# Kernel optimization log

Measured on AMD Instinct MI355X. Metric: run time of the kernel, lower is better.

The kernel has to match this reference:

```python
import jax, jax.numpy as jnp
import numpy as np

B, N, D, K = 16, 65536, 24, 512
ATTRACTION_WEIGHT = 1.0
REPULSION_WEIGHT = 1.5
MARGIN_WEIGHT = 5.0
THRESHOLD = 0.5
MARGIN = 0.2
TAU = 0.7


def setup_inputs() -> dict:
    key = jax.random.key(0)
    k1, k2, k3 = jax.random.split(key, 3)
    beta = jax.random.normal(k1, (B, N, 1), jnp.float32)
    embed = jax.random.normal(k2, (B, N, D), jnp.float32)
    # First K hits of each event are the condensation points (one per instance),
    # remaining hits get a random instance id in [0, K).
    rand_sid = jax.random.randint(k3, (B, N - K), 0, K, jnp.int32)
    cp_sid = jnp.broadcast_to(jnp.arange(K, dtype=jnp.int32), (B, K))
    slice_id = jnp.concatenate([cp_sid, rand_sid], axis=1)
    is_cp = jnp.concatenate(
        [jnp.ones((B, K), jnp.int32), jnp.zeros((B, N - K), jnp.int32)], axis=1)
    return {"beta": beta, "embed": embed, "slice_id": slice_id, "is_cp": is_cp}


def _per_batch(beta_b, emb_b, sid, cp):
    # beta_b: [N], emb_b: [N, D], sid: [N] int, cp: [N] int
    n = beta_b.shape[0]
    f32 = beta_b.dtype
    cp_mask = cp == 1
    pos_count = cp_mask.sum()
    neg_count = n - pos_count

    seg_cnt = jax.ops.segment_sum(jnp.ones((n,), f32), sid, num_segments=K)
    inst_present = seg_cnt > 0
    cp_per_inst = jax.ops.segment_sum(cp_mask.astype(f32), sid, num_segments=K)
    valid_inst = inst_present & (cp_per_inst == 1)  # inst_cp.sum() == 1

    # --- grouped softmax CE over each instance (temperature TAU) ---
    logits = jnp.clip(beta_b, -20.0, 20.0) / TAU
    seg_max = jax.ops.segment_max(logits, sid, num_segments=K)
    safe_max = jnp.where(inst_present, seg_max, 0.0)
    ex = jnp.exp(logits - safe_max[sid])
    denom = jax.ops.segment_sum(ex, sid, num_segments=K)
    cp_logit = jax.ops.segment_sum(jnp.where(cp_mask, logits, 0.0), sid,
                                   num_segments=K)  # exactly one cp when valid
    p_cp = jnp.exp(cp_logit - safe_max) / jnp.maximum(denom, 1e-30)
    loss_inst = -jnp.log(p_cp + 1e-9)
    slice_count = valid_inst.sum()
    beta_slice_ce = jnp.where(valid_inst, loss_inst, 0.0).sum() / jnp.maximum(slice_count, 1)

    # --- margin loss on sigmoid(beta) ---
    beta_prob = jax.nn.sigmoid(jnp.clip(beta_b, -20.0, 20.0))
    pos_m = jnp.where(cp_mask, jax.nn.relu(THRESHOLD + MARGIN - beta_prob), 0.0).sum() \
        / jnp.maximum(pos_count, 1)
    neg_m = jnp.where(cp_mask, 0.0, jax.nn.relu(beta_prob - (THRESHOLD - MARGIN))).sum() \
        / jnp.maximum(neg_count, 1)
    beta_loss = beta_slice_ce + MARGIN_WEIGHT * (pos_m + neg_m)

    # --- attraction: hits pulled to first CP of their instance ---
    idx = jnp.arange(n, dtype=jnp.int32)
    first_cp = jax.ops.segment_min(jnp.where(cp_mask, idx, n), sid, num_segments=K)
    has_cp = (first_cp < n) & inst_present
    cp_emb = emb_b[jnp.minimum(first_cp, n - 1)]  # [K, D]
    d2 = jnp.minimum(((emb_b - cp_emb[sid]) ** 2).sum(-1), 50.0)
    d2_mean = jax.ops.segment_sum(d2, sid, num_segments=K) / jnp.maximum(seg_cnt, 1.0)
    attraction = ATTRACTION_WEIGHT * jnp.where(has_cp, d2_mean, 0.0).sum()

    # --- repulsion: pairwise exp(-d2) between CP embeddings (incl. diagonal) ---
    m = has_cp.astype(f32)
    mcount = m.sum()
    sq = (cp_emb ** 2).sum(-1)
    pd2 = sq[:, None] + sq[None, :] - 2.0 * (cp_emb @ cp_emb.T)
    pd2 = jnp.clip(pd2, 0.0, 50.0)
    rep = (jnp.exp(-pd2) * (m[:, None] * m[None, :])).sum() / jnp.maximum(mcount * mcount, 1.0)
    repulsion = jnp.where(mcount > 1, REPULSION_WEIGHT * rep, 0.0)

    valid = (pos_count >= 1) & (neg_count >= 1) & (slice_count > 0)
    total = beta_loss + attraction + repulsion
    return total, beta_loss, attraction, repulsion, valid


def reference(beta, embed, slice_id, is_cp):
    beta = jnp.nan_to_num(jnp.squeeze(beta, -1), nan=0.0, posinf=0.0, neginf=0.0)
    embed = jnp.nan_to_num(embed, nan=0.0, posinf=0.0, neginf=0.0)
    total, bl, al, rl, valid = jax.vmap(_per_batch)(beta, embed, slice_id, is_cp)
    v = valid.astype(beta.dtype)
    count = v.sum()
    safe = jnp.maximum(count, 1.0)
    ok = count > 0
    final = jnp.where(ok, (total * v).sum() / safe, 0.0)
    beta_log = jnp.where(ok, (bl * v).sum() / safe, 0.0)
    attr_log = jnp.where(ok, (al * v).sum() / safe, 0.0)
    repl_log = jnp.where(ok, (rl * v).sum() / safe, 0.0)
    return final, beta_log, attr_log, repl_log
```

## Files before the change

kernel.cpp:

```cpp
#include <hip/hip_runtime.h>
#include <math.h>

#define BB 16
#define NN 65536
#define DD 24
#define KK 512
#define CH 64
#define HPB (NN / CH)
#define TPB 256
#define RPB 4
#define GB (KK / RPB)

__device__ __forceinline__ float fixnum(float v) {
  return __builtin_isfinite(v) ? v : 0.0f;
}

__device__ __forceinline__ float blockReduceSum(float v, float* sbuf) {
  __syncthreads();
  #pragma unroll
  for (int off = 32; off > 0; off >>= 1) v += __shfl_down(v, off, 64);
  int wid = threadIdx.x >> 6, lane = threadIdx.x & 63;
  if (lane == 0) sbuf[wid] = v;
  __syncthreads();
  return sbuf[0] + sbuf[1] + sbuf[2] + sbuf[3];
}

__global__ __launch_bounds__(TPB) void k1_seg(
    const float* __restrict__ beta, const int* __restrict__ sid,
    const int* __restrict__ iscp,
    float* __restrict__ cnt_part, float* __restrict__ den_part,
    float* __restrict__ cp_cnt, float* __restrict__ cp_logit,
    int* __restrict__ first_cp, float* __restrict__ margin)
{
  __shared__ float s_cnt[KK];
  __shared__ float s_den[KK];
  __shared__ float sred[4];
  int b = blockIdx.x / CH, c = blockIdx.x % CH, t = threadIdx.x;
  for (int k = t; k < KK; k += TPB) { s_cnt[k] = 0.f; s_den[k] = 0.f; }
  __syncthreads();
  float pm = 0.f, nm = 0.f;
  #pragma unroll
  for (int i = 0; i < HPB / TPB; ++i) {
    int h = c * HPB + i * TPB + t;
    size_t g = (size_t)b * NN + h;
    float bv = fixnum(beta[g]);
    float bc = fminf(fmaxf(bv, -20.f), 20.f);
    float logit = bc / 0.7f;
    int s = sid[g];
    atomicAdd(&s_cnt[s], 1.0f);
    atomicAdd(&s_den[s], expf(logit));
    float prob = 1.0f / (1.0f + expf(-bc));
    if (iscp[g] == 1) {
      atomicAdd(&cp_cnt[b * KK + s], 1.0f);
      atomicAdd(&cp_logit[b * KK + s], logit);
      atomicMin(&first_cp[b * KK + s], h);
      pm += fmaxf(0.7f - prob, 0.f);
    } else {
      nm += fmaxf(prob - 0.3f, 0.f);
    }
  }
  float pms = blockReduceSum(pm, sred);
  float nms = blockReduceSum(nm, sred);
  if (t == 0) { atomicAdd(&margin[2 * b], pms); atomicAdd(&margin[2 * b + 1], nms); }
  __syncthreads();
  for (int k = t; k < KK; k += TPB) {
    cnt_part[((size_t)b * CH + c) * KK + k] = s_cnt[k];
    den_part[((size_t)b * CH + c) * KK + k] = s_den[k];
  }
}

__global__ __launch_bounds__(TPB) void k2_fin(
    const float* __restrict__ embed,
    const float* __restrict__ cnt_part, const float* __restrict__ den_part,
    const float* __restrict__ cp_cnt, const float* __restrict__ cp_logit,
    const int* __restrict__ first_cp,
    float* __restrict__ seg_cnt, float* __restrict__ loss_v,
    float* __restrict__ valid_f, float* __restrict__ has_cp_f,
    float* __restrict__ cp_emb)
{
  int idx = blockIdx.x * TPB + threadIdx.x;
  if (idx >= BB * KK) return;
  int b = idx / KK, k = idx - b * KK;
  float cnt = 0.f, den = 0.f;
  for (int c = 0; c < CH; ++c) {
    cnt += cnt_part[((size_t)b * CH + c) * KK + k];
    den += den_part[((size_t)b * CH + c) * KK + k];
  }
  bool present = cnt > 0.f;
  bool vinst = present && (cp_cnt[idx] == 1.0f);
  float p = expf(cp_logit[idx]) / fmaxf(den, 1e-30f);
  float loss = -logf(p + 1e-9f);
  loss_v[idx] = vinst ? loss : 0.f;
  valid_f[idx] = vinst ? 1.f : 0.f;
  int fc = first_cp[idx];
  has_cp_f[idx] = ((fc < NN) && present) ? 1.f : 0.f;
  seg_cnt[idx] = cnt;
  int row = fc < NN ? fc : NN - 1;
  const float4* src = (const float4*)(embed + ((size_t)b * NN + row) * DD);
  float4* dst = (float4*)(cp_emb + (size_t)idx * DD);
  #pragma unroll
  for (int q = 0; q < DD / 4; ++q) {
    float4 v = src[q];
    v.x = fixnum(v.x); v.y = fixnum(v.y); v.z = fixnum(v.z); v.w = fixnum(v.w);
    dst[q] = v;
  }
}

__global__ __launch_bounds__(TPB) void k3_attr(
    const float* __restrict__ embed, const int* __restrict__ sid,
    const float* __restrict__ cp_emb, float* __restrict__ d2_part)
{
  __shared__ float s_ce[KK * DD];
  __shared__ float s_d2[KK];
  int b = blockIdx.x / CH, c = blockIdx.x % CH, t = threadIdx.x;
  const float4* src = (const float4*)(cp_emb + (size_t)b * KK * DD);
  float4* dst = (float4*)s_ce;
  for (int i = t; i < KK * DD / 4; i += TPB) dst[i] = src[i];
  for (int k = t; k < KK; k += TPB) s_d2[k] = 0.f;
  __syncthreads();
  #pragma unroll
  for (int i = 0; i < HPB / TPB; ++i) {
    int h = c * HPB + i * TPB + t;
    size_t g = (size_t)b * NN + h;
    const float4* e = (const float4*)(embed + g * DD);
    int s = sid[g];
    const float4* ce = (const float4*)(s_ce + s * DD);
    float d2 = 0.f;
    #pragma unroll
    for (int q = 0; q < DD / 4; ++q) {
      float4 ev = e[q]; float4 cv = ce[q];
      float x;
      x = fixnum(ev.x) - cv.x; d2 += x * x;
      x = fixnum(ev.y) - cv.y; d2 += x * x;
      x = fixnum(ev.z) - cv.z; d2 += x * x;
      x = fixnum(ev.w) - cv.w; d2 += x * x;
    }
    atomicAdd(&s_d2[s], fminf(d2, 50.f));
  }
  __syncthreads();
  for (int k = t; k < KK; k += TPB)
    d2_part[((size_t)b * CH + c) * KK + k] = s_d2[k];
}

__global__ __launch_bounds__(TPB) void k3b_rep(
    const float* __restrict__ cp_emb, const float* __restrict__ has_cp_f,
    float* __restrict__ rep_sum)
{
  __shared__ float sred[4];
  int b = blockIdx.x / GB;
  int r0 = (blockIdx.x % GB) * RPB;
  int t = threadIdx.x;
  int j0 = t, j1 = t + TPB;
  const float* base = cp_emb + (size_t)b * KK * DD;
  float cj0[DD], cj1[DD];
  #pragma unroll
  for (int d = 0; d < DD; ++d) { cj0[d] = base[j0 * DD + d]; cj1[d] = base[j1 * DD + d]; }
  float m0 = has_cp_f[b * KK + j0], m1 = has_cp_f[b * KK + j1];
  float acc = 0.f;
  for (int ri = 0; ri < RPB; ++ri) {
    int i = r0 + ri;
    float mi = has_cp_f[b * KK + i];
    float d20 = 0.f, d21 = 0.f;
    #pragma unroll
    for (int d = 0; d < DD; ++d) {
      float ci = base[i * DD + d];
      float x0 = ci - cj0[d]; d20 += x0 * x0;
      float x1 = ci - cj1[d]; d21 += x1 * x1;
    }
    acc += mi * (m0 * expf(-fminf(d20, 50.f)) + m1 * expf(-fminf(d21, 50.f)));
  }
  float tot = blockReduceSum(acc, sred);
  if (t == 0) atomicAdd(&rep_sum[b], tot);
}

__global__ __launch_bounds__(TPB) void k4_batch(
    const float* __restrict__ d2_part, const float* __restrict__ seg_cnt,
    const float* __restrict__ loss_v, const float* __restrict__ valid_f,
    const float* __restrict__ cp_cnt, const float* __restrict__ has_cp_f,
    const float* __restrict__ margin, const float* __restrict__ rep_sum,
    float* __restrict__ batch_out)
{
  __shared__ float sred[4];
  int b = blockIdx.x, t = threadIdx.x;
  float attr = 0.f, ce = 0.f, vcnt = 0.f, pcnt = 0.f, mcnt = 0.f;
  for (int k = t; k < KK; k += TPB) {
    float ds = 0.f;
    for (int c = 0; c < CH; ++c) ds += d2_part[((size_t)b * CH + c) * KK + k];
    int idx = b * KK + k;
    float cnt = seg_cnt[idx];
    float hc = has_cp_f[idx];
    attr += hc * (ds / fmaxf(cnt, 1.f));
    ce += loss_v[idx];
    vcnt += valid_f[idx];
    pcnt += cp_cnt[idx];
    mcnt += hc;
  }
  attr = blockReduceSum(attr, sred);
  ce   = blockReduceSum(ce, sred);
  vcnt = blockReduceSum(vcnt, sred);
  pcnt = blockReduceSum(pcnt, sred);
  mcnt = blockReduceSum(mcnt, sred);
  if (t == 0) {
    float pos = pcnt, neg = (float)NN - pos;
    float slice_ce = ce / fmaxf(vcnt, 1.f);
    float pm = margin[2 * b] / fmaxf(pos, 1.f);
    float nm = margin[2 * b + 1] / fmaxf(neg, 1.f);
    float beta_loss = slice_ce + 5.0f * (pm + nm);
    float rep = rep_sum[b] / fmaxf(mcnt * mcnt, 1.f);
    float repulsion = (mcnt > 1.f) ? 1.5f * rep : 0.f;
    float valid = (pos >= 1.f && neg >= 1.f && vcnt > 0.f) ? 1.f : 0.f;
    batch_out[b * 8 + 0] = beta_loss + attr + repulsion;
    batch_out[b * 8 + 1] = beta_loss;
    batch_out[b * 8 + 2] = attr;
    batch_out[b * 8 + 3] = repulsion;
    batch_out[b * 8 + 4] = valid;
  }
}

__global__ void k5_final(const float* __restrict__ batch_out, float* __restrict__ out) {
  if (threadIdx.x == 0 && blockIdx.x == 0) {
    float s0 = 0.f, s1 = 0.f, s2 = 0.f, s3 = 0.f, c = 0.f;
    for (int b = 0; b < BB; ++b) {
      float v = batch_out[b * 8 + 4];
      c  += v;
      s0 += batch_out[b * 8 + 0] * v;
      s1 += batch_out[b * 8 + 1] * v;
      s2 += batch_out[b * 8 + 2] * v;
      s3 += batch_out[b * 8 + 3] * v;
    }
    float safe = fmaxf(c, 1.f);
    bool ok = c > 0.f;
    out[0] = ok ? s0 / safe : 0.f;
    out[1] = ok ? s1 / safe : 0.f;
    out[2] = ok ? s2 / safe : 0.f;
    out[3] = ok ? s3 / safe : 0.f;
  }
}

extern "C" void kernel_launch(void* const* d_in, const int* in_sizes, int n_in,
                              void* d_out, int out_size, void* d_ws, size_t ws_size,
                              hipStream_t stream) {
  (void)in_sizes; (void)n_in; (void)out_size; (void)ws_size;
  const float* beta  = (const float*)d_in[0];
  const float* embed = (const float*)d_in[1];
  const int*   sid   = (const int*)d_in[2];
  const int*   iscp  = (const int*)d_in[3];
  float* out = (float*)d_out;
  char* ws = (char*)d_ws;

  size_t off = 0;
  auto alloc = [&](size_t bytes) {
    size_t o = off; off += (bytes + 255) & ~(size_t)255; return o;
  };
  const size_t BKf = (size_t)BB * KK * 4;
  size_t o_cp_cnt  = alloc(BKf);
  size_t o_cp_lg   = alloc(BKf);
  size_t o_margin  = alloc((size_t)BB * 2 * 4);
  size_t o_rep     = alloc((size_t)BB * 4);
  size_t zero_end  = off;
  size_t o_first   = alloc(BKf);
  size_t o_cnt_p   = alloc((size_t)BB * CH * KK * 4);
  size_t o_den_p   = alloc((size_t)BB * CH * KK * 4);
  size_t o_d2_p    = alloc((size_t)BB * CH * KK * 4);
  size_t o_cpe     = alloc((size_t)BB * KK * DD * 4);
  size_t o_segc    = alloc(BKf);
  size_t o_lossv   = alloc(BKf);
  size_t o_validf  = alloc(BKf);
  size_t o_hascp   = alloc(BKf);
  size_t o_bout    = alloc((size_t)BB * 8 * 4);

  hipMemsetAsync(ws, 0, zero_end, stream);
  hipMemsetAsync(ws + o_first, 0x7f, BKf, stream);

  k1_seg<<<BB * CH, TPB, 0, stream>>>(beta, sid, iscp,
      (float*)(ws + o_cnt_p), (float*)(ws + o_den_p),
      (float*)(ws + o_cp_cnt), (float*)(ws + o_cp_lg),
      (int*)(ws + o_first), (float*)(ws + o_margin));

  k2_fin<<<(BB * KK) / TPB, TPB, 0, stream>>>(embed,
      (const float*)(ws + o_cnt_p), (const float*)(ws + o_den_p),
      (const float*)(ws + o_cp_cnt), (const float*)(ws + o_cp_lg),
      (const int*)(ws + o_first),
      (float*)(ws + o_segc), (float*)(ws + o_lossv), (float*)(ws + o_validf),
      (float*)(ws + o_hascp), (float*)(ws + o_cpe));

  k3_attr<<<BB * CH, TPB, 0, stream>>>(embed, sid,
      (const float*)(ws + o_cpe), (float*)(ws + o_d2_p));

  k3b_rep<<<BB * GB, TPB, 0, stream>>>((const float*)(ws + o_cpe),
      (const float*)(ws + o_hascp), (float*)(ws + o_rep));

  k4_batch<<<BB, TPB, 0, stream>>>((const float*)(ws + o_d2_p),
      (const float*)(ws + o_segc), (const float*)(ws + o_lossv),
      (const float*)(ws + o_validf), (const float*)(ws + o_cp_cnt),
      (const float*)(ws + o_hascp), (const float*)(ws + o_margin),
      (const float*)(ws + o_rep), (float*)(ws + o_bout));

  k5_final<<<1, 64, 0, stream>>>((const float*)(ws + o_bout), out);
}
```

Before: 244.3 us.

## Fuse attraction and repulsion kernels, drop memsets and global atomics

```diff
diff --git a/kernel.cpp b/kernel.cpp
--- a/kernel.cpp
+++ b/kernel.cpp
@@ -8,8 +8,7 @@
 #define CH 64
 #define HPB (NN / CH)
 #define TPB 256
-#define RPB 4
-#define GB (KK / RPB)
+#define RPB 8
 
 __device__ __forceinline__ float fixnum(float v) {
   return __builtin_isfinite(v) ? v : 0.0f;
@@ -28,32 +27,39 @@
 __global__ __launch_bounds__(TPB) void k1_seg(
     const float* __restrict__ beta, const int* __restrict__ sid,
     const int* __restrict__ iscp,
-    float* __restrict__ cnt_part, float* __restrict__ den_part,
-    float* __restrict__ cp_cnt, float* __restrict__ cp_logit,
-    int* __restrict__ first_cp, float* __restrict__ margin)
+    float* __restrict__ cnt_p, float* __restrict__ den_p,
+    float* __restrict__ cpc_p, float* __restrict__ cpl_p,
+    int* __restrict__ first_p, float* __restrict__ marg_p)
 {
-  __shared__ float s_cnt[KK];
-  __shared__ float s_den[KK];
+  __shared__ float s_cnt[KK], s_den[KK], s_cpc[KK], s_cpl[KK];
+  __shared__ int   s_first[KK];
   __shared__ float sred[4];
-  int b = blockIdx.x / CH, c = blockIdx.x % CH, t = threadIdx.x;
-  for (int k = t; k < KK; k += TPB) { s_cnt[k] = 0.f; s_den[k] = 0.f; }
-  __syncthreads();
+  int b = blockIdx.x >> 6, c = blockIdx.x & 63, t = threadIdx.x;
+  for (int k = t; k < KK; k += TPB) {
+    s_cnt[k] = 0.f; s_den[k] = 0.f; s_cpc[k] = 0.f; s_cpl[k] = 0.f; s_first[k] = NN;
+  }
+  __syncthreads();
+  int h0 = c * HPB + t * 4;
+  size_t g0 = (size_t)b * NN + h0;
+  float4 bv = *(const float4*)(beta + g0);
+  int4   sv = *(const int4*)(sid + g0);
+  int4   cv = *(const int4*)(iscp + g0);
   float pm = 0.f, nm = 0.f;
-  #pragma unroll
-  for (int i = 0; i < HPB / TPB; ++i) {
-    int h = c * HPB + i * TPB + t;
-    size_t g = (size_t)b * NN + h;
-    float bv = fixnum(beta[g]);
-    float bc = fminf(fmaxf(bv, -20.f), 20.f);
-    float logit = bc / 0.7f;
-    int s = sid[g];
+  float bs[4] = {bv.x, bv.y, bv.z, bv.w};
+  int   ss[4] = {sv.x, sv.y, sv.z, sv.w};
+  int   cs[4] = {cv.x, cv.y, cv.z, cv.w};
+  #pragma unroll
+  for (int j = 0; j < 4; ++j) {
+    float bc = fminf(fmaxf(fixnum(bs[j]), -20.f), 20.f);
+    float logit = bc * (1.0f / 0.7f);
+    int s = ss[j];
     atomicAdd(&s_cnt[s], 1.0f);
-    atomicAdd(&s_den[s], expf(logit));
-    float prob = 1.0f / (1.0f + expf(-bc));
-    if (iscp[g] == 1) {
-      atomicAdd(&cp_cnt[b * KK + s], 1.0f);
-      atomicAdd(&cp_logit[b * KK + s], logit);
-      atomicMin(&first_cp[b * KK + s], h);
+    atomicAdd(&s_den[s], __expf(logit));
+    float prob = 1.0f / (1.0f + __expf(-bc));
+    if (cs[j] == 1) {
+      atomicAdd(&s_cpc[s], 1.0f);
+      atomicAdd(&s_cpl[s], logit);
+      atomicMin(&s_first[s], h0 + j);
       pm += fmaxf(0.7f - prob, 0.f);
     } else {
       nm += fmaxf(prob - 0.3f, 0.f);
@@ -61,40 +67,47 @@
   }
   float pms = blockReduceSum(pm, sred);
   float nms = blockReduceSum(nm, sred);
-  if (t == 0) { atomicAdd(&margin[2 * b], pms); atomicAdd(&margin[2 * b + 1], nms); }
-  __syncthreads();
+  if (t == 0) { marg_p[2 * blockIdx.x] = pms; marg_p[2 * blockIdx.x + 1] = nms; }
+  __syncthreads();
+  size_t base = ((size_t)b * CH + c) * KK;
   for (int k = t; k < KK; k += TPB) {
-    cnt_part[((size_t)b * CH + c) * KK + k] = s_cnt[k];
-    den_part[((size_t)b * CH + c) * KK + k] = s_den[k];
+    cnt_p[base + k] = s_cnt[k]; den_p[base + k] = s_den[k];
+    cpc_p[base + k] = s_cpc[k]; cpl_p[base + k] = s_cpl[k];
+    first_p[base + k] = s_first[k];
   }
 }
 
 __global__ __launch_bounds__(TPB) void k2_fin(
     const float* __restrict__ embed,
-    const float* __restrict__ cnt_part, const float* __restrict__ den_part,
-    const float* __restrict__ cp_cnt, const float* __restrict__ cp_logit,
-    const int* __restrict__ first_cp,
+    const float* __restrict__ cnt_p, const float* __restrict__ den_p,
+    const float* __restrict__ cpc_p, const float* __restrict__ cpl_p,
+    const int* __restrict__ first_p,
     float* __restrict__ seg_cnt, float* __restrict__ loss_v,
     float* __restrict__ valid_f, float* __restrict__ has_cp_f,
-    float* __restrict__ cp_emb)
+    float* __restrict__ cpc_tot, float* __restrict__ cp_emb,
+    float* __restrict__ d2_acc, float* __restrict__ rep_acc)
 {
   int idx = blockIdx.x * TPB + threadIdx.x;
-  if (idx >= BB * KK) return;
-  int b = idx / KK, k = idx - b * KK;
-  float cnt = 0.f, den = 0.f;
+  int b = idx >> 9, k = idx & (KK - 1);
+  float cnt = 0.f, den = 0.f, cpc = 0.f, cpl = 0.f;
+  int fc = NN;
+  #pragma unroll 8
   for (int c = 0; c < CH; ++c) {
-    cnt += cnt_part[((size_t)b * CH + c) * KK + k];
-    den += den_part[((size_t)b * CH + c) * KK + k];
+    size_t base = ((size_t)b * CH + c) * KK + k;
+    cnt += cnt_p[base]; den += den_p[base];
+    cpc += cpc_p[base]; cpl += cpl_p[base];
+    fc = min(fc, first_p[base]);
   }
   bool present = cnt > 0.f;
-  bool vinst = present && (cp_cnt[idx] == 1.0f);
-  float p = expf(cp_logit[idx]) / fmaxf(den, 1e-30f);
-  float loss = -logf(p + 1e-9f);
-  loss_v[idx] = vinst ? loss : 0.f;
+  bool vinst = present && (cpc == 1.0f);
+  float p = __expf(cpl) / fmaxf(den, 1e-30f);
+  seg_cnt[idx] = cnt;
+  cpc_tot[idx] = cpc;
+  loss_v[idx] = vinst ? -__logf(p + 1e-9f) : 0.f;
   valid_f[idx] = vinst ? 1.f : 0.f;
-  int fc = first_cp[idx];
   has_cp_f[idx] = ((fc < NN) && present) ? 1.f : 0.f;
-  seg_cnt[idx] = cnt;
+  d2_acc[idx] = 0.f;
+  if (idx < BB) rep_acc[idx] = 0.f;
   int row = fc < NN ? fc : NN - 1;
   const float4* src = (const float4*)(embed + ((size_t)b * NN + row) * DD);
   float4* dst = (float4*)(cp_emb + (size_t)idx * DD);
@@ -106,25 +119,24 @@
   }
 }
 
-__global__ __launch_bounds__(TPB) void k3_attr(
+__global__ __launch_bounds__(TPB) void k3_attr_rep(
     const float* __restrict__ embed, const int* __restrict__ sid,
-    const float* __restrict__ cp_emb, float* __restrict__ d2_part)
+    const float* __restrict__ cp_emb, const float* __restrict__ has_cp_f,
+    float* __restrict__ d2_acc, float* __restrict__ rep_acc)
 {
-  __shared__ float s_ce[KK * DD];
   __shared__ float s_d2[KK];
-  int b = blockIdx.x / CH, c = blockIdx.x % CH, t = threadIdx.x;
-  const float4* src = (const float4*)(cp_emb + (size_t)b * KK * DD);
-  float4* dst = (float4*)s_ce;
-  for (int i = t; i < KK * DD / 4; i += TPB) dst[i] = src[i];
+  __shared__ float sred[4];
+  int b = blockIdx.x >> 6, c = blockIdx.x & 63, t = threadIdx.x;
   for (int k = t; k < KK; k += TPB) s_d2[k] = 0.f;
   __syncthreads();
+  const float* cebase = cp_emb + (size_t)b * KK * DD;
   #pragma unroll
   for (int i = 0; i < HPB / TPB; ++i) {
     int h = c * HPB + i * TPB + t;
     size_t g = (size_t)b * NN + h;
-    const float4* e = (const float4*)(embed + g * DD);
     int s = sid[g];
-    const float4* ce = (const float4*)(s_ce + s * DD);
+    const float4* e  = (const float4*)(embed + g * DD);
+    const float4* ce = (const float4*)(cebase + (size_t)s * DD);
     float d2 = 0.f;
     #pragma unroll
     for (int q = 0; q < DD / 4; ++q) {
@@ -139,97 +151,92 @@
   }
   __syncthreads();
   for (int k = t; k < KK; k += TPB)
-    d2_part[((size_t)b * CH + c) * KK + k] = s_d2[k];
-}
-
-__global__ __launch_bounds__(TPB) void k3b_rep(
-    const float* __restrict__ cp_emb, const float* __restrict__ has_cp_f,
-    float* __restrict__ rep_sum)
-{
-  __shared__ float sred[4];
-  int b = blockIdx.x / GB;
-  int r0 = (blockIdx.x % GB) * RPB;
-  int t = threadIdx.x;
+    atomicAdd(&d2_acc[b * KK + k], s_d2[k]);
+
   int j0 = t, j1 = t + TPB;
-  const float* base = cp_emb + (size_t)b * KK * DD;
   float cj0[DD], cj1[DD];
-  #pragma unroll
-  for (int d = 0; d < DD; ++d) { cj0[d] = base[j0 * DD + d]; cj1[d] = base[j1 * DD + d]; }
+  const float4* cj0p = (const float4*)(cebase + (size_t)j0 * DD);
+  const float4* cj1p = (const float4*)(cebase + (size_t)j1 * DD);
+  #pragma unroll
+  for (int q = 0; q < DD / 4; ++q) {
+    float4 a = cj0p[q], bq = cj1p[q];
+    cj0[q*4] = a.x; cj0[q*4+1] = a.y; cj0[q*4+2] = a.z; cj0[q*4+3] = a.w;
+    cj1[q*4] = bq.x; cj1[q*4+1] = bq.y; cj1[q*4+2] = bq.z; cj1[q*4+3] = bq.w;
+  }
   float m0 = has_cp_f[b * KK + j0], m1 = has_cp_f[b * KK + j1];
   float acc = 0.f;
+  #pragma unroll
   for (int ri = 0; ri < RPB; ++ri) {
-    int i = r0 + ri;
+    int i = c * RPB + ri;
     float mi = has_cp_f[b * KK + i];
     float d20 = 0.f, d21 = 0.f;
     #pragma unroll
     for (int d = 0; d < DD; ++d) {
-      float ci = base[i * DD + d];
+      float ci = cebase[i * DD + d];
       float x0 = ci - cj0[d]; d20 += x0 * x0;
       float x1 = ci - cj1[d]; d21 += x1 * x1;
     }
-    acc += mi * (m0 * expf(-fminf(d20, 50.f)) + m1 * expf(-fminf(d21, 50.f)));
+    acc += mi * (m0 * __expf(-fminf(d20, 50.f)) + m1 * __expf(-fminf(d21, 50.f)));
   }
   float tot = blockReduceSum(acc, sred);
-  if (t == 0) atomicAdd(&rep_sum[b], tot);
-}
-
-__global__ __launch_bounds__(TPB) void k4_batch(
-    const float* __restrict__ d2_part, const float* __restrict__ seg_cnt,
+  if (t == 0) atomicAdd(&rep_acc[b], tot);
+}
+
+__global__ __launch_bounds__(1024) void k4_final(
+    const float* __restrict__ d2_acc, const float* __restrict__ seg_cnt,
     const float* __restrict__ loss_v, const float* __restrict__ valid_f,
-    const float* __restrict__ cp_cnt, const float* __restrict__ has_cp_f,
-    const float* __restrict__ margin, const float* __restrict__ rep_sum,
-    float* __restrict__ batch_out)
+    const float* __restrict__ cpc_tot, const float* __restrict__ has_cp_f,
+    const float* __restrict__ marg_p, const float* __restrict__ rep_acc,
+    float* __restrict__ out)
 {
-  __shared__ float sred[4];
-  int b = blockIdx.x, t = threadIdx.x;
+  __shared__ float s_b[BB][5];
+  int w = threadIdx.x >> 6, l = threadIdx.x & 63;
+  int b = w;
   float attr = 0.f, ce = 0.f, vcnt = 0.f, pcnt = 0.f, mcnt = 0.f;
-  for (int k = t; k < KK; k += TPB) {
-    float ds = 0.f;
-    for (int c = 0; c < CH; ++c) ds += d2_part[((size_t)b * CH + c) * KK + k];
+  #pragma unroll
+  for (int k = l; k < KK; k += 64) {
     int idx = b * KK + k;
-    float cnt = seg_cnt[idx];
     float hc = has_cp_f[idx];
-    attr += hc * (ds / fmaxf(cnt, 1.f));
-    ce += loss_v[idx];
+    attr += hc * (d2_acc[idx] / fmaxf(seg_cnt[idx], 1.f));
+    ce   += loss_v[idx];
     vcnt += valid_f[idx];
-    pcnt += cp_cnt[idx];
+    pcnt += cpc_tot[idx];
     mcnt += hc;
   }
-  attr = blockReduceSum(attr, sred);
-  ce   = blockReduceSum(ce, sred);
-  vcnt = blockReduceSum(vcnt, sred);
-  pcnt = blockReduceSum(pcnt, sred);
-  mcnt = blockReduceSum(mcnt, sred);
-  if (t == 0) {
+  float pm = marg_p[(b * CH + l) * 2];
+  float nm = marg_p[(b * CH + l) * 2 + 1];
+  #pragma unroll
+  for (int off = 32; off > 0; off >>= 1) {
+    attr += __shfl_down(attr, off, 64);
+    ce   += __shfl_down(ce, off, 64);
+    vcnt += __shfl_down(vcnt, off, 64);
+    pcnt += __shfl_down(pcnt, off, 64);
+    mcnt += __shfl_down(mcnt, off, 64);
+    pm   += __shfl_down(pm, off, 64);
+    nm   += __shfl_down(nm, off, 64);
+  }
+  if (l == 0) {
     float pos = pcnt, neg = (float)NN - pos;
     float slice_ce = ce / fmaxf(vcnt, 1.f);
-    float pm = margin[2 * b] / fmaxf(pos, 1.f);
-    float nm = margin[2 * b + 1] / fmaxf(neg, 1.f);
-    float beta_loss = slice_ce + 5.0f * (pm + nm);
-    float rep = rep_sum[b] / fmaxf(mcnt * mcnt, 1.f);
+    float beta_loss = slice_ce + 5.0f * (pm / fmaxf(pos, 1.f) + nm / fmaxf(neg, 1.f));
+    float rep = rep_acc[b] / fmaxf(mcnt * mcnt, 1.f);
     float repulsion = (mcnt > 1.f) ? 1.5f * rep : 0.f;
-    float valid = (pos >= 1.f && neg >= 1.f && vcnt > 0.f) ? 1.f : 0.f;
-    batch_out[b * 8 + 0] = beta_loss + attr + repulsion;
-    batch_out[b * 8 + 1] = beta_loss;
-    batch_out[b * 8 + 2] = attr;
-    batch_out[b * 8 + 3] = repulsion;
-    batch_out[b * 8 + 4] = valid;
-  }
-}
-
-__global__ void k5_final(const float* __restrict__ batch_out, float* __restrict__ out) {
-  if (threadIdx.x == 0 && blockIdx.x == 0) {
-    float s0 = 0.f, s1 = 0.f, s2 = 0.f, s3 = 0.f, c = 0.f;
-    for (int b = 0; b < BB; ++b) {
-      float v = batch_out[b * 8 + 4];
-      c  += v;
-      s0 += batch_out[b * 8 + 0] * v;
-      s1 += batch_out[b * 8 + 1] * v;
-      s2 += batch_out[b * 8 + 2] * v;
-      s3 += batch_out[b * 8 + 3] * v;
+    float v = (pos >= 1.f && neg >= 1.f && vcnt > 0.f) ? 1.f : 0.f;
+    s_b[w][0] = (beta_loss + attr + repulsion) * v;
+    s_b[w][1] = beta_loss * v;
+    s_b[w][2] = attr * v;
+    s_b[w][3] = repulsion * v;
+    s_b[w][4] = v;
+  }
+  __syncthreads();
+  if (threadIdx.x == 0) {
+    float s0 = 0.f, s1 = 0.f, s2 = 0.f, s3 = 0.f, cv = 0.f;
+    #pragma unroll
+    for (int i = 0; i < BB; ++i) {
+      s0 += s_b[i][0]; s1 += s_b[i][1]; s2 += s_b[i][2]; s3 += s_b[i][3]; cv += s_b[i][4];
     }
-    float safe = fmaxf(c, 1.f);
-    bool ok = c > 0.f;
+    float safe = fmaxf(cv, 1.f);
+    bool ok = cv > 0.f;
     out[0] = ok ? s0 / safe : 0.f;
     out[1] = ok ? s1 / safe : 0.f;
     out[2] = ok ? s2 / safe : 0.f;
@@ -252,49 +259,43 @@
   auto alloc = [&](size_t bytes) {
     size_t o = off; off += (bytes + 255) & ~(size_t)255; return o;
   };
+  const size_t BCK = (size_t)BB * CH * KK * 4;
   const size_t BKf = (size_t)BB * KK * 4;
-  size_t o_cp_cnt  = alloc(BKf);
-  size_t o_cp_lg   = alloc(BKf);
-  size_t o_margin  = alloc((size_t)BB * 2 * 4);
-  size_t o_rep     = alloc((size_t)BB * 4);
-  size_t zero_end  = off;
-  size_t o_first   = alloc(BKf);
-  size_t o_cnt_p   = alloc((size_t)BB * CH * KK * 4);
-  size_t o_den_p   = alloc((size_t)BB * CH * KK * 4);
-  size_t o_d2_p    = alloc((size_t)BB * CH * KK * 4);
-  size_t o_cpe     = alloc((size_t)BB * KK * DD * 4);
-  size_t o_segc    = alloc(BKf);
-  size_t o_lossv   = alloc(BKf);
-  size_t o_validf  = alloc(BKf);
-  size_t o_hascp   = alloc(BKf);
-  size_t o_bout    = alloc((size_t)BB * 8 * 4);
-
-  hipMemsetAsync(ws, 0, zero_end, stream);
-  hipMemsetAsync(ws + o_first, 0x7f, BKf, stream);
+  size_t o_cnt_p  = alloc(BCK);
+  size_t o_den_p  = alloc(BCK);
+  size_t o_cpc_p  = alloc(BCK);
+  size_t o_cpl_p  = alloc(BCK);
+  size_t o_first  = alloc(BCK);
+  size_t o_marg   = alloc((size_t)BB * CH * 2 * 4);
+  size_t o_segc   = alloc(BKf);
+  size_t o_lossv  = alloc(BKf);
+  size_t o_validf = alloc(BKf);
+  size_t o_hascp  = alloc(BKf);
+  size_t o_cpct   = alloc(BKf);
+  size_t o_d2     = alloc(BKf);
+  size_t o_cpe    = alloc((size_t)BB * KK * DD * 4);
+  size_t o_rep    = alloc((size_t)BB * 4);
 
   k1_seg<<<BB * CH, TPB, 0, stream>>>(beta, sid, iscp,
       (float*)(ws + o_cnt_p), (float*)(ws + o_den_p),
-      (float*)(ws + o_cp_cnt), (float*)(ws + o_cp_lg),
-      (int*)(ws + o_first), (float*)(ws + o_margin));
+      (float*)(ws + o_cpc_p), (float*)(ws + o_cpl_p),
+      (int*)(ws + o_first), (float*)(ws + o_marg));
 
   k2_fin<<<(BB * KK) / TPB, TPB, 0, stream>>>(embed,
       (const float*)(ws + o_cnt_p), (const float*)(ws + o_den_p),
-      (const float*)(ws + o_cp_cnt), (const float*)(ws + o_cp_lg),
+      (const float*)(ws + o_cpc_p), (const float*)(ws + o_cpl_p),
       (const int*)(ws + o_first),
       (float*)(ws + o_segc), (float*)(ws + o_lossv), (float*)(ws + o_validf),
-      (float*)(ws + o_hascp), (float*)(ws + o_cpe));
-
-  k3_attr<<<BB * CH, TPB, 0, stream>>>(embed, sid,
-      (const float*)(ws + o_cpe), (float*)(ws + o_d2_p));
-
-  k3b_rep<<<BB * GB, TPB, 0, stream>>>((const float*)(ws + o_cpe),
-      (const float*)(ws + o_hascp), (float*)(ws + o_rep));
-
-  k4_batch<<<BB, TPB, 0, stream>>>((const float*)(ws + o_d2_p),
+      (float*)(ws + o_hascp), (float*)(ws + o_cpct), (float*)(ws + o_cpe),
+      (float*)(ws + o_d2), (float*)(ws + o_rep));
+
+  k3_attr_rep<<<BB * CH, TPB, 0, stream>>>(embed, sid,
+      (const float*)(ws + o_cpe), (const float*)(ws + o_hascp),
+      (float*)(ws + o_d2), (float*)(ws + o_rep));
+
+  k4_final<<<1, 1024, 0, stream>>>((const float*)(ws + o_d2),
       (const float*)(ws + o_segc), (const float*)(ws + o_lossv),
-      (const float*)(ws + o_validf), (const float*)(ws + o_cp_cnt),
-      (const float*)(ws + o_hascp), (const float*)(ws + o_margin),
-      (const float*)(ws + o_rep), (float*)(ws + o_bout));
-
-  k5_final<<<1, 64, 0, stream>>>((const float*)(ws + o_bout), out);
-}
+      (const float*)(ws + o_validf), (const float*)(ws + o_cpct),
+      (const float*)(ws + o_hascp), (const float*)(ws + o_marg),
+      (const float*)(ws + o_rep), out);
+}
```

Measured after the change: 200.3 us. 1.22x faster.
